# Performance work log

Measured on AMD Instinct MI355X. Metric: run time of the kernel, lower is better.

## Reference

```python
import jax, jax.numpy as jnp
import numpy as np

DIM = 64
HEADS = 2
HD = DIM // HEADS          # 32
ALPHA = 4.0
KS = 5                     # dwc kernel size
MLP_H = 4 * DIM            # 256
LN_EPS = 1e-5


def layernorm(x, g, b):
    mu = jnp.mean(x, axis=-1, keepdims=True)
    var = jnp.mean(jnp.square(x - mu), axis=-1, keepdims=True)
    return (x - mu) * jax.lax.rsqrt(var + LN_EPS) * g + b


def safe_pow(x, p):
    # relu(x) ** p with well-defined value (and grad) at x <= 0
    xr = jnp.maximum(x, 0.0)
    safe = jnp.where(xr > 0, xr, 1.0)
    return jnp.where(xr > 0, safe ** p, 0.0)


def block_forward(x, H, W, ln1_g, ln1_b, w_qg, w_kv, pos_enc, scale_p, power_p,
                  dwc_w, dwc_b, w_proj, b_proj, ln2_g, ln2_b, w_fc1, b_fc1, w_fc2, b_fc2):
    B, N, C = x.shape
    h1 = layernorm(x, ln1_g, ln1_b)

    qg = h1 @ w_qg                         # [B,N,2C]
    q, gate = qg[..., :C], qg[..., C:]
    kv = h1 @ w_kv                         # [B,N,2C] (sr_ratio==1)
    k, v = kv[..., :C], kv[..., C:]
    k = k + pos_enc                        # [1,N,C]

    scale = jax.nn.softplus(scale_p)       # [1,1,C]
    power = 1.0 + ALPHA * jax.nn.sigmoid(power_p)  # [1,h,1,hd]
    q = q / scale
    k = k / scale

    # [B, h, N, hd]
    q = q.reshape(B, N, HEADS, HD).transpose(0, 2, 1, 3)
    k = k.reshape(B, N, HEADS, HD).transpose(0, 2, 1, 3)
    v = v.reshape(B, N, HEADS, HD).transpose(0, 2, 1, 3)

    q_pos = safe_pow(q, power)
    q_neg = safe_pow(-q, power)
    k_pos = safe_pow(k, power)
    k_neg = safe_pow(-k, power)

    q_sim = jnp.concatenate([q_pos, q_neg], axis=-1)   # [B,h,N,2hd]
    q_opp = jnp.concatenate([q_neg, q_pos], axis=-1)
    k_cat = jnp.concatenate([k_pos, k_neg], axis=-1)

    v1, v2 = v[..., :HD // 2], v[..., HD // 2:]

    n = N  # n_reduced == N for sr_ratio==1
    inv_sqrt_n = jnp.float32(n) ** -0.5
    k_mean = jnp.mean(k_cat, axis=-2)                  # [B,h,2hd]

    z_sim = 1.0 / (jnp.einsum('bhnd,bhd->bhn', q_sim, k_mean)[..., None] + 1e-6)
    kv_sim = jnp.einsum('bhnd,bhne->bhde', k_cat * inv_sqrt_n, v1 * inv_sqrt_n)
    x_sim = jnp.einsum('bhnd,bhde->bhne', q_sim, kv_sim) * z_sim

    z_opp = 1.0 / (jnp.einsum('bhnd,bhd->bhn', q_opp, k_mean)[..., None] + 1e-6)
    kv_opp = jnp.einsum('bhnd,bhne->bhde', k_cat * inv_sqrt_n, v2 * inv_sqrt_n)
    x_opp = jnp.einsum('bhnd,bhde->bhne', q_opp, kv_opp) * z_opp

    xa = jnp.concatenate([x_sim, x_opp], axis=-1)      # [B,h,N,hd]
    xa = xa.transpose(0, 2, 1, 3).reshape(B, N, C)

    # depthwise 5x5 conv over v in image layout
    v_img = v.reshape(B * HEADS, n, HD).transpose(0, 2, 1).reshape(B * HEADS, HD, H, W)
    v_dwc = jax.lax.conv_general_dilated(
        v_img, dwc_w, window_strides=(1, 1), padding='SAME',
        feature_group_count=HD, dimension_numbers=('NCHW', 'OIHW', 'NCHW'))
    v_dwc = v_dwc + dwc_b[None, :, None, None]
    v_dwc = v_dwc.reshape(B, C, H * W).transpose(0, 2, 1)  # [B,N,C]

    xa = (xa + v_dwc) * gate
    xa = xa @ w_proj + b_proj

    x = x + xa
    h2 = layernorm(x, ln2_g, ln2_b)
    m = jax.nn.gelu(h2 @ w_fc1 + b_fc1, approximate=False) @ w_fc2 + b_fc2
    return x + m


def setup_inputs() -> dict:
    key = jax.random.key(0)
    ks = jax.random.split(key, 12)
    B, H, W = 16, 128, 128
    N = H * W
    s = 0.02
    return {
        'x': jax.random.normal(ks[0], (B, N, DIM), jnp.float32),
        'H': H, 'W': W,
        'ln1_g': jnp.ones((DIM,), jnp.float32),
        'ln1_b': jnp.zeros((DIM,), jnp.float32),
        'w_qg': jax.random.normal(ks[1], (DIM, 2 * DIM), jnp.float32) * s,
        'w_kv': jax.random.normal(ks[2], (DIM, 2 * DIM), jnp.float32) * s,
        'pos_enc': jax.random.normal(ks[3], (1, N, DIM), jnp.float32) * s,
        'scale_p': jax.random.normal(ks[4], (1, 1, DIM), jnp.float32) * s,
        'power_p': jax.random.normal(ks[5], (1, HEADS, 1, HD), jnp.float32) * s,
        'dwc_w': jax.random.normal(ks[6], (HD, 1, KS, KS), jnp.float32) * s,
        'dwc_b': jnp.zeros((HD,), jnp.float32),
        'w_proj': jax.random.normal(ks[7], (DIM, DIM), jnp.float32) * s,
        'b_proj': jnp.zeros((DIM,), jnp.float32),
        'ln2_g': jnp.ones((DIM,), jnp.float32),
        'ln2_b': jnp.zeros((DIM,), jnp.float32),
        'w_fc1': jax.random.normal(ks[8], (DIM, MLP_H), jnp.float32) * s,
        'b_fc1': jnp.zeros((MLP_H,), jnp.float32),
        'w_fc2': jax.random.normal(ks[9], (MLP_H, DIM), jnp.float32) * s,
        'b_fc2': jnp.zeros((DIM,), jnp.float32),
    }


def reference(x, H, W, ln1_g, ln1_b, w_qg, w_kv, pos_enc, scale_p, power_p,
              dwc_w, dwc_b, w_proj, b_proj, ln2_g, ln2_b, w_fc1, b_fc1, w_fc2, b_fc2):
    return block_forward(x, H, W, ln1_g, ln1_b, w_qg, w_kv, pos_enc, scale_p, power_p,
                         dwc_w, dwc_b, w_proj, b_proj, ln2_g, ln2_b, w_fc1, b_fc1, w_fc2, b_fc2)
```

## Files before the change

kernel.cpp:

```cpp
#include <hip/hip_runtime.h>
#include <hip/hip_bf16.h>

#define NB 16
#define NT 16384
#define NTOK (NB * NT)

typedef __hip_bfloat16 bf16;
typedef __attribute__((ext_vector_type(8))) short short8;
typedef __attribute__((ext_vector_type(4))) float f32x4;

static __device__ __forceinline__ f32x4 MFMA(short8 a, short8 b, f32x4 c) {
    return __builtin_amdgcn_mfma_f32_16x16x32_bf16(a, b, c, 0, 0, 0);
}
static __device__ __forceinline__ short bfs(float f) {
    union { bf16 h; short s; } u; u.h = __float2bfloat16(f); return u.s;
}
static __device__ __forceinline__ float sbf(short s) {
    union { bf16 h; short s; } u; u.s = s; return __bfloat162float(u.h);
}
static __device__ __forceinline__ bf16 f2bf(float v) { return __float2bfloat16(v); }
static __device__ __forceinline__ float us2f(unsigned short u) {
    union { unsigned int i; float f; } x; x.i = ((unsigned int)u) << 16; return x.f;
}

static __device__ __forceinline__ float safe_pow(float x, float p) {
    return (x > 0.f) ? __builtin_amdgcn_exp2f(p * __builtin_amdgcn_logf(x)) : 0.f;
}
static __device__ __forceinline__ float sigm(float y) {
    return __builtin_amdgcn_rcpf(1.f + __builtin_amdgcn_exp2f(-1.44269504f * y));
}

static __device__ __forceinline__ int swb(int row, int tok) {
    return row * 64 + ((tok * 2) ^ (((row >> 1) & 3) << 4));
}

__global__ __launch_bounds__(256)
void k0_prep(const float* __restrict__ w_qg, const float* __restrict__ w_kv,
             const float* __restrict__ w_fc1, const float* __restrict__ w_fc2,
             short* __restrict__ wqk_f, short* __restrict__ wf1_f, short* __restrict__ wf2_f)
{
    int idx = blockIdx.x * 256 + threadIdx.x;
    if (idx < 16384) {
        int k = idx >> 8, col = idx & 255;
        float wv = (col < 128) ? w_qg[k * 128 + col] : w_kv[k * 128 + col - 128];
        int ct = col >> 4, ks = k >> 5, lane = (col & 15) + 16 * ((k & 31) >> 3), j = k & 7;
        wqk_f[((ct * 2 + ks) * 64 + lane) * 8 + j] = bfs(wv);
    } else if (idx < 32768) {
        int i2 = idx - 16384, k = i2 >> 8, col = i2 & 255;
        int ct = col >> 4, ks = k >> 5, lane = (col & 15) + 16 * ((k & 31) >> 3), j = k & 7;
        wf1_f[((ct * 2 + ks) * 64 + lane) * 8 + j] = bfs(w_fc1[k * 256 + col]);
    } else if (idx < 49152) {
        int i2 = idx - 32768, k = i2 >> 6, col = i2 & 63;
        int ct2 = col >> 4, ks = k >> 5, lane = (col & 15) + 16 * ((k & 31) >> 3), j = k & 7;
        wf2_f[((ct2 * 8 + ks) * 64 + lane) * 8 + j] = bfs(w_fc2[k * 64 + col]);
    }
}

__global__ __launch_bounds__(256)
void k1_proj(const float* __restrict__ x,
             const float* __restrict__ ln1_g, const float* __restrict__ ln1_b,
             const short* __restrict__ wqk_f,
             const float* __restrict__ pos_enc,
             const float* __restrict__ scale_p, const float* __restrict__ power_p,
             bf16* __restrict__ qb, bf16* __restrict__ gbuf, bf16* __restrict__ vbuf,
             float* __restrict__ km_g, float* __restrict__ kv_g)
{
    __shared__ __align__(16) unsigned char lds[49152];
    __shared__ __align__(16) short wqk_s[16384];
    const int tid = threadIdx.x;
    const int b = blockIdx.y, chunk = blockIdx.x;
    const int w = tid >> 6, l = tid & 63, l15 = l & 15, g = l >> 4;
    unsigned char* kft = lds + w * 12288;
    unsigned char* vt  = kft + 8192;

    #pragma unroll
    for (int i = 0; i < 8; ++i)
        ((uint4*)wqk_s)[tid * 8 + i] = ((const uint4*)wqk_f)[tid * 8 + i];

    float g1v[16], b1v[16];
    #pragma unroll
    for (int j = 0; j < 8; j++) {
        g1v[j]     = ln1_g[g * 8 + j];      b1v[j]     = ln1_b[g * 8 + j];
        g1v[8 + j] = ln1_g[32 + g * 8 + j]; b1v[8 + j] = ln1_b[32 + g * 8 + j];
    }
    float isc[4], pwk[4];
    #pragma unroll
    for (int ct = 0; ct < 4; ct++) {
        int ch = l15 + 16 * ct;
        float s = scale_p[ch];
        float sp = 0.69314718f * __builtin_amdgcn_logf(1.f + __builtin_amdgcn_exp2f(1.44269504f * s));
        isc[ct] = __builtin_amdgcn_rcpf(sp);
        pwk[ct] = 1.f + 4.f * sigm(power_p[ch]);
    }

    f32x4 acc[2][2][4];
    #pragma unroll
    for (int s = 0; s < 2; s++)
        #pragma unroll
        for (int h = 0; h < 2; h++)
            #pragma unroll
            for (int mt = 0; mt < 4; mt++) { f32x4 z = {0.f,0.f,0.f,0.f}; acc[s][h][mt] = z; }
    float kmp[4] = {0.f,0.f,0.f,0.f}, kmn[4] = {0.f,0.f,0.f,0.f};

    __syncthreads();

    for (int it = 0; it < 8; ++it) {
        const int tok0 = chunk * 512 + (it * 4 + w) * 16;
        const size_t rowb = (size_t)b * NT + tok0;
        const float* xrow = x + (rowb + l15) * 64;
        float4 t0 = *(const float4*)(xrow + g * 8);
        float4 t1 = *(const float4*)(xrow + g * 8 + 4);
        float4 t2 = *(const float4*)(xrow + 32 + g * 8);
        float4 t3 = *(const float4*)(xrow + 32 + g * 8 + 4);
        float xa8[8] = {t0.x,t0.y,t0.z,t0.w,t1.x,t1.y,t1.z,t1.w};
        float xb8[8] = {t2.x,t2.y,t2.z,t2.w,t3.x,t3.y,t3.z,t3.w};
        float s1 = 0.f, s2 = 0.f;
        #pragma unroll
        for (int j = 0; j < 8; j++) {
            s1 += xa8[j] + xb8[j];
            s2 += xa8[j] * xa8[j] + xb8[j] * xb8[j];
        }
        s1 += __shfl_xor(s1, 16, 64); s1 += __shfl_xor(s1, 32, 64);
        s2 += __shfl_xor(s2, 16, 64); s2 += __shfl_xor(s2, 32, 64);
        float mu = s1 * 0.015625f;
        float var = s2 * 0.015625f - mu * mu;
        float rs = rsqrtf(var + 1e-5f);
        short8 A0, A1;
        #pragma unroll
        for (int j = 0; j < 8; j++) {
            A0[j] = bfs((xa8[j] - mu) * rs * g1v[j] + b1v[j]);
            A1[j] = bfs((xb8[j] - mu) * rs * g1v[8 + j] + b1v[8 + j]);
        }
        const int tokp = (it & 1) * 16;
        #pragma unroll
        for (int ct = 0; ct < 16; ct++) {
            short8 f0 = *(const short8*)(wqk_s + (ct * 2 + 0) * 512 + l * 8);
            short8 f1 = *(const short8*)(wqk_s + (ct * 2 + 1) * 512 + l * 8);
            f32x4 c = {0.f,0.f,0.f,0.f};
            c = MFMA(A0, f0, c);
            c = MFMA(A1, f1, c);
            if (ct < 4) {
                #pragma unroll
                for (int r = 0; r < 4; r++)
                    qb[(rowb + g * 4 + r) * 64 + l15 + 16 * ct] = f2bf(c[r] * isc[ct]);
            } else if (ct < 8) {
                #pragma unroll
                for (int r = 0; r < 4; r++)
                    gbuf[(rowb + g * 4 + r) * 64 + l15 + 16 * (ct - 4)] = f2bf(c[r]);
            } else if (ct < 12) {
                const int ctk = ct - 8, kchan = l15 + 16 * ctk;
                const int hh = kchan >> 5, d = kchan & 31;
                #pragma unroll
                for (int r = 0; r < 4; r++) {
                    int n = tok0 + g * 4 + r;
                    float kvl = (c[r] + pos_enc[(size_t)n * 64 + kchan]) * isc[ctk];
                    float kp = safe_pow(kvl, pwk[ctk]);
                    float kn = safe_pow(-kvl, pwk[ctk]);
                    kmp[ctk] += kp; kmn[ctk] += kn;
                    int tk = tokp + g * 4 + r;
                    *(short*)(kft + swb(hh * 64 + d, tk))      = bfs(kp);
                    *(short*)(kft + swb(hh * 64 + 32 + d, tk)) = bfs(kn);
                }
            } else {
                const int ctv = ct - 12, vchan = l15 + 16 * ctv;
                const int hh = vchan >> 5, vc = vchan & 31;
                #pragma unroll
                for (int r = 0; r < 4; r++) {
                    int tk = tokp + g * 4 + r;
                    vbuf[(rowb + g * 4 + r) * 64 + vchan] = f2bf(c[r]);
                    *(short*)(vt + swb(hh * 32 + vc, tk)) = bfs(c[r]);
                }
            }
        }
        if (it & 1) {
            #pragma unroll
            for (int h = 0; h < 2; h++) {
                int rv0 = h * 32 + l15, rv1 = h * 32 + 16 + l15;
                short8 Bv0 = *(const short8*)(vt + rv0 * 64 + ((g * 16) ^ (((rv0 >> 1) & 3) << 4)));
                short8 Bv1 = *(const short8*)(vt + rv1 * 64 + ((g * 16) ^ (((rv1 >> 1) & 3) << 4)));
                #pragma unroll
                for (int mt = 0; mt < 4; mt++) {
                    int rk = h * 64 + mt * 16 + l15;
                    short8 Ak = *(const short8*)(kft + rk * 64 + ((g * 16) ^ (((rk >> 1) & 3) << 4)));
                    acc[0][h][mt] = MFMA(Ak, Bv0, acc[0][h][mt]);
                    acc[1][h][mt] = MFMA(Ak, Bv1, acc[1][h][mt]);
                }
            }
        }
    }
    const float invN = 1.f / 16384.f;
    float* kvb = kv_g + (size_t)b * 4096;
    #pragma unroll
    for (int s = 0; s < 2; s++)
        #pragma unroll
        for (int h = 0; h < 2; h++)
            #pragma unroll
            for (int mt = 0; mt < 4; mt++)
                #pragma unroll
                for (int r = 0; r < 4; r++)
                    atomicAdd(&kvb[((s * 2 + h) * 64 + mt * 16 + g * 4 + r) * 16 + l15],
                              acc[s][h][mt][r] * invN);
    #pragma unroll
    for (int ct = 0; ct < 4; ct++) {
        kmp[ct] += __shfl_xor(kmp[ct], 16, 64); kmp[ct] += __shfl_xor(kmp[ct], 32, 64);
        kmn[ct] += __shfl_xor(kmn[ct], 16, 64); kmn[ct] += __shfl_xor(kmn[ct], 32, 64);
    }
    if (g == 0) {
        #pragma unroll
        for (int ct = 0; ct < 4; ct++) {
            int kchan = l15 + 16 * ct, hh = kchan >> 5, d = kchan & 31;
            atomicAdd(&km_g[b * 128 + hh * 64 + d],      kmp[ct] * invN);
            atomicAdd(&km_g[b * 128 + hh * 64 + 32 + d], kmn[ct] * invN);
        }
    }
}

__global__ __launch_bounds__(256)
void k2_dwc(const bf16* __restrict__ vbuf,
            const float* __restrict__ dwc_w, const float* __restrict__ dwc_b,
            bf16* __restrict__ vdb)
{
    __shared__ __align__(16) unsigned short tile[12][36][64];
    const int tid = threadIdx.x;
    const int b = blockIdx.y;
    const int ty = blockIdx.x >> 2, tx = blockIdx.x & 3;
    const int y0 = ty * 8, x0 = tx * 32;

    #pragma unroll
    for (int i = 0; i < 27; ++i) {
        int cid = i * 256 + tid;
        int yy = cid / 576;
        int rem = cid - yy * 576;
        int xx = rem >> 4;
        int c4 = rem & 15;
        int Y = y0 - 2 + yy, X = x0 - 2 + xx;
        uint2 val = make_uint2(0u, 0u);
        if ((unsigned)Y < 128u && (unsigned)X < 128u)
            val = *(const uint2*)(vbuf + (((size_t)b * NT + Y * 128 + X) * 64 + c4 * 4));
        *(uint2*)(&tile[yy][xx][c4 * 4]) = val;
    }
    __syncthreads();

    const int w = tid >> 6, c = tid & 63, d = c & 31;
    float wt[25];
    #pragma unroll
    for (int k = 0; k < 25; k++) wt[k] = dwc_w[d * 25 + k];
    const float bias = dwc_b[d];

    #pragma unroll
    for (int yl2 = 0; yl2 < 2; ++yl2) {
        const int yl = w * 2 + yl2;
        float cw[5][5];
        #pragma unroll
        for (int xx = 0; xx < 4; ++xx)
            #pragma unroll
            for (int ky = 0; ky < 5; ++ky)
                cw[ky][xx] = us2f(tile[yl + ky][xx][c]);
        #pragma unroll
        for (int xl = 0; xl < 32; ++xl) {
            const int jn = (xl + 4) % 5;
            #pragma unroll
            for (int ky = 0; ky < 5; ++ky)
                cw[ky][jn] = us2f(tile[yl + ky][xl + 4][c]);
            float acc = bias;
            #pragma unroll
            for (int ky = 0; ky < 5; ++ky)
                #pragma unroll
                for (int kx = 0; kx < 5; ++kx)
                    acc += wt[ky * 5 + kx] * cw[ky][(xl + kx) % 5];
            const int Y = y0 + yl, X = x0 + xl;
            vdb[((size_t)b * NT + Y * 128 + X) * 64 + c] = f2bf(acc);
        }
    }
}

__global__ __launch_bounds__(1024, 4)
void k3_main(const float* __restrict__ x,
             const bf16* __restrict__ qb, const bf16* __restrict__ gbuf, const bf16* __restrict__ vdb,
             const float* __restrict__ km_g, const float* __restrict__ kv_g,
             const float* __restrict__ power_p,
             const float* __restrict__ w_proj, const float* __restrict__ b_proj,
             const float* __restrict__ ln2_g, const float* __restrict__ ln2_b,
             const short* __restrict__ wf1_f, const short* __restrict__ wf2_f,
             const float* __restrict__ b_fc1, const float* __restrict__ b_fc2,
             float* __restrict__ out)
{
    __shared__ __align__(16) short wkv_s[8][512];
    __shared__ __align__(16) short wp_s[8][512];
    __shared__ __align__(16) short wf1_s[16384];
    __shared__ __align__(16) short wf2_s[16384];
    __shared__ __align__(16) unsigned char tbuf[16][2048];

    const int tid = threadIdx.x, b = blockIdx.y, chunk = blockIdx.x;
    const int w = tid >> 6, l = tid & 63, l15 = l & 15, g = l >> 4;
    unsigned char* tb = tbuf[w];

    if (tid < 512) {
        int frag = tid >> 6, lane = tid & 63;
        int s2h = frag >> 1, ks = frag & 1;
        short8 v;
        #pragma unroll
        for (int j = 0; j < 8; ++j) {
            int idx = s2h * 1024 + (ks * 32 + (lane >> 4) * 8 + j) * 16 + (lane & 15);
            v[j] = bfs(kv_g[(size_t)b * 4096 + idx]);
        }
        *(short8*)&wkv_s[frag][lane * 8] = v;
    } else {
        int t2 = tid - 512;
        int frag = t2 >> 6, lane = t2 & 63;
        int ct = frag >> 1, ks = frag & 1;
        short8 v;
        #pragma unroll
        for (int j = 0; j < 8; ++j) {
            int idx = (ks * 32 + (lane >> 4) * 8 + j) * 64 + ct * 16 + (lane & 15);
            v[j] = bfs(w_proj[idx]);
        }
        *(short8*)&wp_s[frag][lane * 8] = v;
    }
    #pragma unroll
    for (int i = 0; i < 2; ++i) {
        ((uint4*)wf1_s)[tid * 2 + i] = ((const uint4*)wf1_f)[tid * 2 + i];
        ((uint4*)wf2_s)[tid * 2 + i] = ((const uint4*)wf2_f)[tid * 2 + i];
    }

    short8 Kden[2][2];
    #pragma unroll
    for (int h = 0; h < 2; ++h)
        #pragma unroll
        for (int f = 0; f < 2; ++f)
            #pragma unroll
            for (int j = 0; j < 8; ++j) {
                int d = g * 8 + j;
                float v = 0.f;
                if (l15 == 0)      v = km_g[b * 128 + h * 64 + (f ? 32 + d : d)];
                else if (l15 == 1) v = km_g[b * 128 + h * 64 + (f ? d : 32 + d)];
                Kden[h][f][j] = bfs(v);
            }

    float pw3[2][8];
    #pragma unroll
    for (int h = 0; h < 2; h++)
        #pragma unroll
        for (int j = 0; j < 8; j++)
            pw3[h][j] = 1.f + 4.f * sigm(power_p[h * 32 + g * 8 + j]);
    float bpj[4], g2[4], b2[4], bfc2v[4];
    #pragma unroll
    for (int ct = 0; ct < 4; ct++) {
        int ch = l15 + 16 * ct;
        bpj[ct] = b_proj[ch]; g2[ct] = ln2_g[ch]; b2[ct] = ln2_b[ch]; bfc2v[ct] = b_fc2[ch];
    }
    float bf1v[16];
    #pragma unroll
    for (int ct = 0; ct < 16; ct++) bf1v[ct] = b_fc1[ct * 16 + l15];

    __syncthreads();

    for (int it = 0; it < 2; ++it) {
        const int tok0 = chunk * 512 + (it * 16 + w) * 16;
        const size_t rowb = (size_t)b * NT + tok0;
        const size_t goff = (rowb + l15) * 64;

        short8 q8[2], vd8[2], g8[2];
        #pragma unroll
        for (int ks = 0; ks < 2; ks++) {
            q8[ks]  = *(const short8*)((const short*)qb   + goff + ks * 32 + g * 8);
            vd8[ks] = *(const short8*)((const short*)vdb  + goff + ks * 32 + g * 8);
            g8[ks]  = *(const short8*)((const short*)gbuf + goff + ks * 32 + g * 8);
        }
        float xv[4][4];
        #pragma unroll
        for (int ct = 0; ct < 4; ct++)
            #pragma unroll
            for (int r = 0; r < 4; r++)
                xv[ct][r] = x[(rowb + g * 4 + r) * 64 + l15 + 16 * ct];

        short8 Fqp[2], Fqn[2];
        f32x4 dn[2];
        #pragma unroll
        for (int h = 0; h < 2; h++) {
            #pragma unroll
            for (int j = 0; j < 8; j++) {
                float q = sbf(q8[h][j]);
                Fqp[h][j] = bfs(safe_pow(q, pw3[h][j]));
                Fqn[h][j] = bfs(safe_pow(-q, pw3[h][j]));
            }
            f32x4 z4 = {0.f, 0.f, 0.f, 0.f};
            z4 = MFMA(Fqp[h], Kden[h][0], z4);
            dn[h] = MFMA(Fqn[h], Kden[h][1], z4);
        }

        f32x4 at[4];
        #pragma unroll
        for (int hs = 0; hs < 4; hs++) { f32x4 z4 = {0.f,0.f,0.f,0.f}; at[hs] = z4; }
        #pragma unroll
        for (int h = 0; h < 2; h++) {
            short8 b00 = *(const short8*)&wkv_s[(0 * 2 + h) * 2 + 0][l * 8];
            short8 b01 = *(const short8*)&wkv_s[(0 * 2 + h) * 2 + 1][l * 8];
            short8 b10 = *(const short8*)&wkv_s[(1 * 2 + h) * 2 + 0][l * 8];
            short8 b11 = *(const short8*)&wkv_s[(1 * 2 + h) * 2 + 1][l * 8];
            at[h*2+0] = MFMA(Fqp[h], b00, at[h*2+0]);
            at[h*2+0] = MFMA(Fqn[h], b01, at[h*2+0]);
            at[h*2+1] = MFMA(Fqn[h], b10, at[h*2+1]);
            at[h*2+1] = MFMA(Fqp[h], b11, at[h*2+1]);
        }

        #pragma unroll
        for (int hs = 0; hs < 4; hs++) {
            int h = hs >> 1, s = hs & 1;
            int cb = h * 32 + s * 16;
            #pragma unroll
            for (int r = 0; r < 4; r++) {
                float dv = __shfl(dn[h][r], g * 16 + s, 64);
                float zz = __builtin_amdgcn_rcpf(dv + 1e-6f);
                int tok = g * 4 + r;
                *(short*)(tb + tok * 128 + (((cb + l15) * 2) ^ ((tok & 7) << 4))) = bfs(at[hs][r] * zz);
            }
        }
        short8 Ap[2];
        #pragma unroll
        for (int ks = 0; ks < 2; ks++) {
            short8 t8 = *(short8*)(tb + l15 * 128 + ((ks * 64 + g * 16) ^ ((l15 & 7) << 4)));
            #pragma unroll
            for (int j = 0; j < 8; j++)
                Ap[ks][j] = bfs((sbf(t8[j]) + sbf(vd8[ks][j])) * sbf(g8[ks][j]));
        }

        f32x4 pc[4];
        #pragma unroll
        for (int ct = 0; ct < 4; ct++) {
            short8 w0 = *(const short8*)&wp_s[ct * 2 + 0][l * 8];
            short8 w1 = *(const short8*)&wp_s[ct * 2 + 1][l * 8];
            f32x4 z4 = {0.f,0.f,0.f,0.f};
            z4 = MFMA(Ap[0], w0, z4);
            pc[ct] = MFMA(Ap[1], w1, z4);
        }

        float xm[4][4];
        #pragma unroll
        for (int ct = 0; ct < 4; ct++)
            #pragma unroll
            for (int r = 0; r < 4; r++)
                xm[ct][r] = xv[ct][r] + pc[ct][r] + bpj[ct];
        #pragma unroll
        for (int r = 0; r < 4; r++) {
            float s1 = xm[0][r] + xm[1][r] + xm[2][r] + xm[3][r];
            float s2 = xm[0][r]*xm[0][r] + xm[1][r]*xm[1][r] + xm[2][r]*xm[2][r] + xm[3][r]*xm[3][r];
            #pragma unroll
            for (int m = 1; m < 16; m <<= 1) { s1 += __shfl_xor(s1, m, 64); s2 += __shfl_xor(s2, m, 64); }
            float mu = s1 * 0.015625f;
            float var = s2 * 0.015625f - mu * mu;
            float rs = rsqrtf(var + 1e-5f);
            int tok = g * 4 + r;
            #pragma unroll
            for (int ct = 0; ct < 4; ct++) {
                float h2 = (xm[ct][r] - mu) * rs * g2[ct] + b2[ct];
                *(short*)(tb + tok * 128 + (((ct * 16 + l15) * 2) ^ ((tok & 7) << 4))) = bfs(h2);
            }
        }
        short8 Ah[2];
        #pragma unroll
        for (int ks = 0; ks < 2; ks++)
            Ah[ks] = *(short8*)(tb + l15 * 128 + ((ks * 64 + g * 16) ^ ((l15 & 7) << 4)));

        f32x4 a2[4];
        #pragma unroll
        for (int ct = 0; ct < 4; ct++) { f32x4 z4 = {0.f,0.f,0.f,0.f}; a2[ct] = z4; }
        #pragma unroll
        for (int g4 = 0; g4 < 4; g4++) {
            f32x4 fc[4];
            #pragma unroll
            for (int ctl = 0; ctl < 4; ctl++) {
                int ct = g4 * 4 + ctl;
                short8 f0 = *(const short8*)(wf1_s + (ct * 2 + 0) * 512 + l * 8);
                short8 f1 = *(const short8*)(wf1_s + (ct * 2 + 1) * 512 + l * 8);
                f32x4 z4 = {0.f,0.f,0.f,0.f};
                z4 = MFMA(Ah[0], f0, z4);
                fc[ctl] = MFMA(Ah[1], f1, z4);
            }
            #pragma unroll
            for (int ctl = 0; ctl < 4; ctl++)
                #pragma unroll
                for (int r = 0; r < 4; r++) {
                    float mv = fc[ctl][r] + bf1v[g4 * 4 + ctl];
                    float gl = mv * __builtin_amdgcn_rcpf(1.f +
                        __builtin_amdgcn_exp2f(mv * (-2.30220825f - 0.10294385f * mv * mv)));
                    int tok = g * 4 + r;
                    *(short*)(tb + tok * 128 + (((ctl * 16 + l15) * 2) ^ ((tok & 7) << 4))) = bfs(gl);
                }
            #pragma unroll
            for (int ksl = 0; ksl < 2; ksl++) {
                short8 Ag = *(short8*)(tb + l15 * 128 + ((ksl * 64 + g * 16) ^ ((l15 & 7) << 4)));
                int ks = g4 * 2 + ksl;
                #pragma unroll
                for (int ct2 = 0; ct2 < 4; ct2++) {
                    short8 wv = *(const short8*)(wf2_s + (ct2 * 8 + ks) * 512 + l * 8);
                    a2[ct2] = MFMA(Ag, wv, a2[ct2]);
                }
            }
        }

        float* tb32 = (float*)tb;
        #pragma unroll
        for (int half = 0; half < 2; ++half) {
            #pragma unroll
            for (int ctl = 0; ctl < 2; ++ctl) {
                int ct = half * 2 + ctl;
                #pragma unroll
                for (int r = 0; r < 4; r++)
                    tb32[(g * 4 + r) * 32 + ctl * 16 + l15] = xm[ct][r] + a2[ct][r] + bfc2v[ct];
            }
            #pragma unroll
            for (int i = 0; i < 2; ++i) {
                f32x4 v = *(f32x4*)&tb32[i * 256 + l * 4];
                __builtin_nontemporal_store(v,
                    (f32x4*)(out + (rowb + i * 8 + (l >> 3)) * 64 + half * 32 + (l & 7) * 4));
            }
        }
    }
}

extern "C" void kernel_launch(void* const* d_in, const int* in_sizes, int n_in,
                              void* d_out, int out_size, void* d_ws, size_t ws_size,
                              hipStream_t stream)
{
    const float* x       = (const float*)d_in[0];
    const float* ln1_g   = (const float*)d_in[3];
    const float* ln1_b   = (const float*)d_in[4];
    const float* w_qg    = (const float*)d_in[5];
    const float* w_kv    = (const float*)d_in[6];
    const float* pos     = (const float*)d_in[7];
    const float* scale_p = (const float*)d_in[8];
    const float* power_p = (const float*)d_in[9];
    const float* dwc_w   = (const float*)d_in[10];
    const float* dwc_b   = (const float*)d_in[11];
    const float* w_proj  = (const float*)d_in[12];
    const float* b_proj  = (const float*)d_in[13];
    const float* ln2_g   = (const float*)d_in[14];
    const float* ln2_b   = (const float*)d_in[15];
    const float* w_fc1   = (const float*)d_in[16];
    const float* b_fc1   = (const float*)d_in[17];
    const float* w_fc2   = (const float*)d_in[18];
    const float* b_fc2   = (const float*)d_in[19];
    float* out = (float*)d_out;

    size_t ntc = (size_t)NTOK * 64;
    bf16* qb   = (bf16*)d_ws;
    bf16* gbuf = qb + ntc;
    bf16* vbuf = gbuf + ntc;
    bf16* vdb  = vbuf + ntc;
    float* km_g = (float*)(vdb + ntc);
    float* kv_g = km_g + (size_t)NB * 128;
    short* wqk_f = (short*)(kv_g + (size_t)NB * 4096);
    short* wf1_f = wqk_f + 16384;
    short* wf2_f = wf1_f + 16384;

    hipMemsetAsync(km_g, 0, ((size_t)NB * 128 + (size_t)NB * 4096) * sizeof(float), stream);

    k0_prep<<<dim3(192), 256, 0, stream>>>(w_qg, w_kv, w_fc1, w_fc2, wqk_f, wf1_f, wf2_f);
    k1_proj<<<dim3(32, NB), 256, 0, stream>>>(x, ln1_g, ln1_b, wqk_f, pos, scale_p, power_p,
                                              qb, gbuf, vbuf, km_g, kv_g);
    k2_dwc<<<dim3(64, NB), 256, 0, stream>>>(vbuf, dwc_w, dwc_b, vdb);
    k3_main<<<dim3(32, NB), 1024, 0, stream>>>(x, qb, gbuf, vdb, km_g, kv_g, power_p,
                                               w_proj, b_proj, ln2_g, ln2_b,
                                               wf1_f, wf2_f, b_fc1, b_fc2, out);
}
```

Measured before the change: 263.7 us.

## Fuse depthwise 5x5 conv into main kernel, drop separate dwc pass

Removes the standalone k2_dwc kernel and its vdb intermediate buffer. Each wave in k3_main now computes the depthwise conv for its 16 tokens straight from global vbuf using a sliding register window, stages the bf16 results in its per-wave LDS scratch, and reads them back in MFMA fragment layout. This saves a kernel launch and one full write and read of the conv output. In exchange, halo rows are re-read from global memory without shared-tile reuse, and the main kernel takes on extra register pressure from the 25 weights and the window.

```diff
diff --git a/kernel.cpp b/kernel.cpp
--- a/kernel.cpp
+++ b/kernel.cpp
@@ -19,9 +19,6 @@
     union { bf16 h; short s; } u; u.s = s; return __bfloat162float(u.h);
 }
 static __device__ __forceinline__ bf16 f2bf(float v) { return __float2bfloat16(v); }
-static __device__ __forceinline__ float us2f(unsigned short u) {
-    union { unsigned int i; float f; } x; x.i = ((unsigned int)u) << 16; return x.f;
-}
 
 static __device__ __forceinline__ float safe_pow(float x, float p) {
     return (x > 0.f) ? __builtin_amdgcn_exp2f(p * __builtin_amdgcn_logf(x)) : 0.f;
@@ -215,68 +212,11 @@
     }
 }
 
-__global__ __launch_bounds__(256)
-void k2_dwc(const bf16* __restrict__ vbuf,
-            const float* __restrict__ dwc_w, const float* __restrict__ dwc_b,
-            bf16* __restrict__ vdb)
-{
-    __shared__ __align__(16) unsigned short tile[12][36][64];
-    const int tid = threadIdx.x;
-    const int b = blockIdx.y;
-    const int ty = blockIdx.x >> 2, tx = blockIdx.x & 3;
-    const int y0 = ty * 8, x0 = tx * 32;
-
-    #pragma unroll
-    for (int i = 0; i < 27; ++i) {
-        int cid = i * 256 + tid;
-        int yy = cid / 576;
-        int rem = cid - yy * 576;
-        int xx = rem >> 4;
-        int c4 = rem & 15;
-        int Y = y0 - 2 + yy, X = x0 - 2 + xx;
-        uint2 val = make_uint2(0u, 0u);
-        if ((unsigned)Y < 128u && (unsigned)X < 128u)
-            val = *(const uint2*)(vbuf + (((size_t)b * NT + Y * 128 + X) * 64 + c4 * 4));
-        *(uint2*)(&tile[yy][xx][c4 * 4]) = val;
-    }
-    __syncthreads();
-
-    const int w = tid >> 6, c = tid & 63, d = c & 31;
-    float wt[25];
-    #pragma unroll
-    for (int k = 0; k < 25; k++) wt[k] = dwc_w[d * 25 + k];
-    const float bias = dwc_b[d];
-
-    #pragma unroll
-    for (int yl2 = 0; yl2 < 2; ++yl2) {
-        const int yl = w * 2 + yl2;
-        float cw[5][5];
-        #pragma unroll
-        for (int xx = 0; xx < 4; ++xx)
-            #pragma unroll
-            for (int ky = 0; ky < 5; ++ky)
-                cw[ky][xx] = us2f(tile[yl + ky][xx][c]);
-        #pragma unroll
-        for (int xl = 0; xl < 32; ++xl) {
-            const int jn = (xl + 4) % 5;
-            #pragma unroll
-            for (int ky = 0; ky < 5; ++ky)
-                cw[ky][jn] = us2f(tile[yl + ky][xl + 4][c]);
-            float acc = bias;
-            #pragma unroll
-            for (int ky = 0; ky < 5; ++ky)
-                #pragma unroll
-                for (int kx = 0; kx < 5; ++kx)
-                    acc += wt[ky * 5 + kx] * cw[ky][(xl + kx) % 5];
-            const int Y = y0 + yl, X = x0 + xl;
-            vdb[((size_t)b * NT + Y * 128 + X) * 64 + c] = f2bf(acc);
-        }
-    }
-}
-
 __global__ __launch_bounds__(1024, 4)
 void k3_main(const float* __restrict__ x,
-             const bf16* __restrict__ qb, const bf16* __restrict__ gbuf, const bf16* __restrict__ vdb,
+             const bf16* __restrict__ qb, const bf16* __restrict__ gbuf,
+             const bf16* __restrict__ vbuf,
+             const float* __restrict__ dwc_w, const float* __restrict__ dwc_b,
              const float* __restrict__ km_g, const float* __restrict__ kv_g,
              const float* __restrict__ power_p,
              const float* __restrict__ w_proj, const float* __restrict__ b_proj,
@@ -337,6 +277,12 @@
                 Kden[h][f][j] = bfs(v);
             }
 
+    const int dch = l & 31;
+    float wt[25];
+    #pragma unroll
+    for (int k = 0; k < 25; k++) wt[k] = dwc_w[dch * 25 + k];
+    const float bias_d = dwc_b[dch];
+
     float pw3[2][8];
     #pragma unroll
     for (int h = 0; h < 2; h++)
@@ -360,12 +306,11 @@
         const size_t rowb = (size_t)b * NT + tok0;
         const size_t goff = (rowb + l15) * 64;
 
-        short8 q8[2], vd8[2], g8[2];
+        short8 q8[2], g8[2];
         #pragma unroll
         for (int ks = 0; ks < 2; ks++) {
-            q8[ks]  = *(const short8*)((const short*)qb   + goff + ks * 32 + g * 8);
-            vd8[ks] = *(const short8*)((const short*)vdb  + goff + ks * 32 + g * 8);
-            g8[ks]  = *(const short8*)((const short*)gbuf + goff + ks * 32 + g * 8);
+            q8[ks] = *(const short8*)((const short*)qb   + goff + ks * 32 + g * 8);
+            g8[ks] = *(const short8*)((const short*)gbuf + goff + ks * 32 + g * 8);
         }
         float xv[4][4];
         #pragma unroll
@@ -373,6 +318,43 @@
             #pragma unroll
             for (int r = 0; r < 4; r++)
                 xv[ct][r] = x[(rowb + g * 4 + r) * 64 + l15 + 16 * ct];
+
+        {
+            const int yy0 = (tok0 & 16383) >> 7;
+            const int xx0 = tok0 & 127;
+            const short* vb = (const short*)vbuf + ((size_t)b * NT) * 64 + l;
+            float cw[5][5];
+            #pragma unroll
+            for (int xx = 0; xx < 4; ++xx)
+                #pragma unroll
+                for (int ky = 0; ky < 5; ++ky) {
+                    int Y = yy0 + ky - 2, X = xx0 + xx - 2;
+                    cw[ky][xx] = ((unsigned)Y < 128u && (unsigned)X < 128u)
+                        ? sbf(vb[(size_t)(Y * 128 + X) * 64]) : 0.f;
+                }
+            #pragma unroll
+            for (int xl = 0; xl < 16; ++xl) {
+                const int jn = (xl + 4) % 5;
+                const int Xn = xx0 + xl + 2;
+                #pragma unroll
+                for (int ky = 0; ky < 5; ++ky) {
+                    int Y = yy0 + ky - 2;
+                    cw[ky][jn] = ((unsigned)Y < 128u && (unsigned)Xn < 128u)
+                        ? sbf(vb[(size_t)(Y * 128 + Xn) * 64]) : 0.f;
+                }
+                float acc = bias_d;
+                #pragma unroll
+                for (int ky = 0; ky < 5; ++ky)
+                    #pragma unroll
+                    for (int kx = 0; kx < 5; ++kx)
+                        acc += wt[ky * 5 + kx] * cw[ky][(xl + kx) % 5];
+                *(short*)(tb + xl * 128 + ((l * 2) ^ ((xl & 7) << 4))) = bfs(acc);
+            }
+        }
+        short8 vd8[2];
+        #pragma unroll
+        for (int ks = 0; ks < 2; ks++)
+            vd8[ks] = *(short8*)(tb + l15 * 128 + ((ks * 64 + g * 16) ^ ((l15 & 7) << 4)));
 
         short8 Fqp[2], Fqn[2];
         f32x4 dn[2];
@@ -547,8 +529,7 @@
     bf16* qb   = (bf16*)d_ws;
     bf16* gbuf = qb + ntc;
     bf16* vbuf = gbuf + ntc;
-    bf16* vdb  = vbuf + ntc;
-    float* km_g = (float*)(vdb + ntc);
+    float* km_g = (float*)(vbuf + ntc);
     float* kv_g = km_g + (size_t)NB * 128;
     short* wqk_f = (short*)(kv_g + (size_t)NB * 4096);
     short* wf1_f = wqk_f + 16384;
@@ -559,8 +540,8 @@
     k0_prep<<<dim3(192), 256, 0, stream>>>(w_qg, w_kv, w_fc1, w_fc2, wqk_f, wf1_f, wf2_f);
     k1_proj<<<dim3(32, NB), 256, 0, stream>>>(x, ln1_g, ln1_b, wqk_f, pos, scale_p, power_p,
                                               qb, gbuf, vbuf, km_g, kv_g);
-    k2_dwc<<<dim3(64, NB), 256, 0, stream>>>(vbuf, dwc_w, dwc_b, vdb);
-    k3_main<<<dim3(32, NB), 1024, 0, stream>>>(x, qb, gbuf, vdb, km_g, kv_g, power_p,
+    k3_main<<<dim3(32, NB), 1024, 0, stream>>>(x, qb, gbuf, vbuf, dwc_w, dwc_b,
+                                               km_g, kv_g, power_p,
                                                w_proj, b_proj, ln2_g, ln2_b,
                                                wf1_f, wf2_f, b_fc1, b_fc2, out);
 }
```

After: 453.5 us. 1.72x slower.
